# Kernel optimization log

Measured on AMD Instinct MI355X. Metric: run time of the kernel, lower is better.

## Reference

```python
import jax, jax.numpy as jnp
import numpy as np

NUM_GROUPS = 8
K = 2


def setup_inputs() -> dict:
    key = jax.random.key(0)
    k1, k2, k3 = jax.random.split(key, 3)
    b, l, d = 4, 4096, 2048
    g, k = NUM_GROUPS, K
    hdg = d // g  # 256
    x = jax.random.normal(k1, (b, l, d), dtype=jnp.float32)
    Wg = jax.random.normal(k2, (d, g), dtype=jnp.float32) * 0.02  # gate (no bias)
    Wm = jax.random.normal(k3, (k * hdg, k * hdg), dtype=jnp.float32) * 0.02  # inner Linear
    bm = jnp.zeros((k * hdg,), dtype=jnp.float32)
    return {"x": x, "Wg": Wg, "Wm": Wm, "bm": bm}


def reference(x, Wg, Wm, bm):
    b, l, d = x.shape
    g, k = NUM_GROUPS, K
    hdg = d // g
    # gate: softmax + topk over groups
    S = jax.nn.softmax(x @ Wg, axis=-1)            # [b, l, g]
    G, I = jax.lax.top_k(S, k)                     # [b, l, k] each
    x4 = x.reshape(b, l, g, hdg)
    # gather selected feature groups
    sel = jnp.take_along_axis(x4, I[..., None], axis=2)  # [b, l, k, hdg]
    h = (G[..., None] * sel).reshape(b, l, k * hdg)
    # inner model (Linear)
    h = h @ Wm + bm
    h = h.reshape(b, l, k, hdg)
    # scatter back into original groups
    bi = jnp.arange(b)[:, None, None]
    li = jnp.arange(l)[None, :, None]
    out = x4.at[bi, li, I].set(h)
    return out.reshape(b, l, d)
```

## Files before the change

kernel.cpp:

```cpp
#include <hip/hip_runtime.h>
#include <hip/hip_bf16.h>

#define NTOK   16384
#define DIM    2048
#define NGRP   8
#define HDG    256
#define NIN    512

typedef float f32x4 __attribute__((ext_vector_type(4)));
typedef short bf16x8 __attribute__((ext_vector_type(8)));

static __device__ __forceinline__ unsigned short f2bf(float f) {
    unsigned int u = __builtin_bit_cast(unsigned int, f);
    u = (u + 0x7fffu + ((u >> 16) & 1u)) >> 16;
    return (unsigned short)u;
}

__global__ __launch_bounds__(256) void prep_wm(const float* __restrict__ Wm,
                                               ushort* __restrict__ WmT) {
    __shared__ float tile[64][65];
    const int bk = blockIdx.x * 64;
    const int bn = blockIdx.y * 64;
    const int t = threadIdx.x;
    const int r = t >> 4;
    const int c = (t & 15) * 4;
#pragma unroll
    for (int i = 0; i < 4; i++) {
        const float4 v = *(const float4*)&Wm[(bk + r + i * 16) * 512 + bn + c];
        tile[r + i * 16][c + 0] = v.x;
        tile[r + i * 16][c + 1] = v.y;
        tile[r + i * 16][c + 2] = v.z;
        tile[r + i * 16][c + 3] = v.w;
    }
    __syncthreads();
#pragma unroll
    for (int i = 0; i < 4; i++) {
        const int n = r + i * 16;
        ushort4 o;
        o.x = f2bf(tile[c + 0][n]);
        o.y = f2bf(tile[c + 1][n]);
        o.z = f2bf(tile[c + 2][n]);
        o.w = f2bf(tile[c + 3][n]);
        *(ushort4*)&WmT[(bn + n) * 512 + bk + c] = o;
    }
}

__global__ __launch_bounds__(256) void gate_kernel(
        const float* __restrict__ x, const float* __restrict__ Wg,
        int* __restrict__ Isel, float* __restrict__ gvals) {
    const int t = threadIdx.x;
    const int lane = t & 63;
    const int wave = t >> 6;
    const int tok0 = blockIdx.x * 8;

    __shared__ float red[8][4][8];

    float wgr[8][8];
#pragma unroll
    for (int j = 0; j < 8; j++) {
        const float4 a = *(const float4*)&Wg[(t * 8 + j) * 8];
        const float4 b = *(const float4*)&Wg[(t * 8 + j) * 8 + 4];
        wgr[j][0] = a.x; wgr[j][1] = a.y; wgr[j][2] = a.z; wgr[j][3] = a.w;
        wgr[j][4] = b.x; wgr[j][5] = b.y; wgr[j][6] = b.z; wgr[j][7] = b.w;
    }

    int4 xa[3][2];
#pragma unroll
    for (int p = 0; p < 2; p++) {
        xa[p][0] = *(const int4*)&x[(tok0 + p) * DIM + t * 8];
        xa[p][1] = *(const int4*)&x[(tok0 + p) * DIM + t * 8 + 4];
    }

    const bool s0 = lane & 1;
    const bool s1 = lane & 2;
    const bool s2 = lane & 4;

#pragma unroll
    for (int tt = 0; tt < 8; tt++) {
        const int slot = tt % 3;
        const float* xr = (const float*)&xa[slot][0];
        float acc[8];
#pragma unroll
        for (int g = 0; g < 8; g++) acc[g] = 0.f;
#pragma unroll
        for (int j = 0; j < 8; j++)
#pragma unroll
            for (int g = 0; g < 8; g++)
                acc[g] = fmaf(xr[j], wgr[j][g], acc[g]);
        if (tt + 2 < 8) {
            const int ps = (tt + 2) % 3;
            xa[ps][0] = *(const int4*)&x[(tok0 + tt + 2) * DIM + t * 8];
            xa[ps][1] = *(const int4*)&x[(tok0 + tt + 2) * DIM + t * 8 + 4];
        }
        float n_[4];
#pragma unroll
        for (int j = 0; j < 4; j++) {
            const float keep = s0 ? acc[2 * j + 1] : acc[2 * j];
            const float send = s0 ? acc[2 * j] : acc[2 * j + 1];
            n_[j] = keep + __shfl_xor(send, 1, 64);
        }
        float m_[2];
#pragma unroll
        for (int j = 0; j < 2; j++) {
            const float keep = s1 ? n_[2 * j + 1] : n_[2 * j];
            const float send = s1 ? n_[2 * j] : n_[2 * j + 1];
            m_[j] = keep + __shfl_xor(send, 2, 64);
        }
        float v;
        {
            const float keep = s2 ? m_[1] : m_[0];
            const float send = s2 ? m_[0] : m_[1];
            v = keep + __shfl_xor(send, 4, 64);
        }
        v += __shfl_xor(v, 8, 64);
        v += __shfl_xor(v, 16, 64);
        v += __shfl_xor(v, 32, 64);
        if (lane < 8) red[tt][wave][lane] = v;
    }
    __syncthreads();

    const int ll = lane & 31;
    const int tok_local = wave * 2 + (lane >> 5);

    float v = red[tok_local][ll >> 3][ll & 7];
    v += __shfl_xor(v, 8, 64);
    v += __shfl_xor(v, 16, 64);
    float c[8];
    c[0] = v;
    c[1] = __shfl_xor(c[0], 1, 64);
    c[2] = __shfl_xor(c[0], 2, 64);
    c[3] = __shfl_xor(c[1], 2, 64);
    c[4] = __shfl_xor(c[0], 4, 64);
    c[5] = __shfl_xor(c[1], 4, 64);
    c[6] = __shfl_xor(c[2], 4, 64);
    c[7] = __shfl_xor(c[3], 4, 64);
    const int gbase = ll & 7;

    float m = c[0];
#pragma unroll
    for (int j = 1; j < 8; j++) m = fmaxf(m, c[j]);
    float sum = 0.f;
#pragma unroll
    for (int j = 0; j < 8; j++) sum += __expf(c[j] - m);
    int i0 = 8; float v0 = -3.4e38f;
#pragma unroll
    for (int j = 0; j < 8; j++) {
        const int g = gbase ^ j;
        if (c[j] > v0 || (c[j] == v0 && g < i0)) { v0 = c[j]; i0 = g; }
    }
    int i1 = 8; float v1 = -3.4e38f;
#pragma unroll
    for (int j = 0; j < 8; j++) {
        const int g = gbase ^ j;
        if (g != i0 && (c[j] > v1 || (c[j] == v1 && g < i1))) { v1 = c[j]; i1 = g; }
    }
    const float inv = 1.0f / sum;
    if (ll == 0) {
        const int tok = tok0 + tok_local;
        int2 sp; sp.x = i0; sp.y = i1;
        *(int2*)&Isel[tok * 2] = sp;
        float2 gp; gp.x = __expf(v0 - m) * inv; gp.y = __expf(v1 - m) * inv;
        *(float2*)&gvals[tok * 2] = gp;
    }
}

__global__ __launch_bounds__(256) void scatter_copy(
        const float* __restrict__ x, const int* __restrict__ Isel,
        const float* __restrict__ gvals, float* __restrict__ out,
        ushort* __restrict__ hbuf) {
    const int wave = threadIdx.x >> 6;
    const int lane = threadIdx.x & 63;
    const int tok = blockIdx.x * 4 + wave;
    const int2 sel = *(const int2*)&Isel[tok * 2];
    const float2 gv = *(const float2*)&gvals[tok * 2];
    float4 v[8];
#pragma unroll
    for (int j = 0; j < 8; j++)
        v[j] = *(const float4*)&x[tok * DIM + j * HDG + lane * 4];
#pragma unroll
    for (int j = 0; j < 8; j++) {
        if (j == sel.x || j == sel.y) {
            const float g = (j == sel.x) ? gv.x : gv.y;
            const int slot = (j == sel.x) ? 0 : 1;
            int2 pk;
            pk.x = (int)f2bf(g * v[j].x) | ((int)f2bf(g * v[j].y) << 16);
            pk.y = (int)f2bf(g * v[j].z) | ((int)f2bf(g * v[j].w) << 16);
            *(int2*)&hbuf[tok * NIN + slot * HDG + lane * 4] = pk;
        } else {
            *(float4*)&out[tok * DIM + j * HDG + lane * 4] = v[j];
        }
    }
}

__global__ __launch_bounds__(256) void gemm_scatter(
        const ushort* __restrict__ h, const ushort* __restrict__ WmT,
        const float* __restrict__ bm, const int* __restrict__ Isel,
        float* __restrict__ out) {
    __shared__ ushort Hs[2][128][40];
    __shared__ ushort Ws[2][128][40];
    const int t = threadIdx.x;
    const int lane = t & 63;
    const int wave = t >> 6;
    const int wn = (wave >> 1) * 64;
    const int wt = (wave & 1) * 64;
    const int n_blk = blockIdx.x * 128;
    const int tok_blk = blockIdx.y * 128;

    const int sr = t >> 2;
    const int sc = (t & 3) * 8;

    const ushort* hp0 = &h[(tok_blk + sr) * 512 + sc];
    const ushort* hp1 = hp0 + 64 * 512;
    const ushort* wp0 = &WmT[(n_blk + sr) * 512 + sc];
    const ushort* wp1 = wp0 + 64 * 512;

    int4 rh0[3], rh1[3], rw0[3], rw1[3];
#pragma unroll
    for (int p = 0; p < 2; p++) {
        const int off = p * 32;
        rh0[p] = *(const int4*)(hp0 + off);
        rh1[p] = *(const int4*)(hp1 + off);
        rw0[p] = *(const int4*)(wp0 + off);
        rw1[p] = *(const int4*)(wp1 + off);
    }

    f32x4 acc[4][4];
#pragma unroll
    for (int i = 0; i < 4; i++)
#pragma unroll
        for (int j = 0; j < 4; j++)
            acc[i][j] = (f32x4){0.f, 0.f, 0.f, 0.f};

    const int fr = lane & 15;
    const int kh = (lane >> 4) * 8;

#pragma unroll
    for (int k = 0; k < 16; ++k) {
        const int b = k & 1;
        const int s = k % 3;
        *(int4*)&Hs[b][sr][sc]      = rh0[s];
        *(int4*)&Hs[b][sr + 64][sc] = rh1[s];
        *(int4*)&Ws[b][sr][sc]      = rw0[s];
        *(int4*)&Ws[b][sr + 64][sc] = rw1[s];
        __syncthreads();
        if (k + 2 < 16) {
            const int s2 = (k + 2) % 3;
            const int off = (k + 2) * 32;
            rh0[s2] = *(const int4*)(hp0 + off);
            rh1[s2] = *(const int4*)(hp1 + off);
            rw0[s2] = *(const int4*)(wp0 + off);
            rw1[s2] = *(const int4*)(wp1 + off);
        }
        bf16x8 av[4], bv[4];
#pragma unroll
        for (int i = 0; i < 4; i++) av[i] = *(const bf16x8*)&Ws[b][wn + i * 16 + fr][kh];
#pragma unroll
        for (int j = 0; j < 4; j++) bv[j] = *(const bf16x8*)&Hs[b][wt + j * 16 + fr][kh];
#pragma unroll
        for (int i = 0; i < 4; i++)
#pragma unroll
            for (int j = 0; j < 4; j++)
                acc[i][j] = __builtin_amdgcn_mfma_f32_16x16x32_bf16(
                    av[i], bv[j], acc[i][j], 0, 0, 0);
    }

    const int rq = (lane >> 4) * 4;
    const int n_base = n_blk + wn;
    const int s = n_base >> 8;
    const int n_off_base = (n_base & 255) + rq;
    float4 bmv[4];
#pragma unroll
    for (int i = 0; i < 4; i++) bmv[i] = *(const float4*)&bm[n_base + i * 16 + rq];
#pragma unroll
    for (int j = 0; j < 4; j++) {
        const int tok = tok_blk + wt + j * 16 + fr;
        const int2 sel = *(const int2*)&Isel[tok * 2];
        const int grp = s ? sel.y : sel.x;
        float* op = &out[tok * DIM + grp * HDG + n_off_base];
#pragma unroll
        for (int i = 0; i < 4; i++) {
            float4 o;
            o.x = acc[i][j][0] + bmv[i].x;
            o.y = acc[i][j][1] + bmv[i].y;
            o.z = acc[i][j][2] + bmv[i].z;
            o.w = acc[i][j][3] + bmv[i].w;
            *(float4*)&op[i * 16] = o;
        }
    }
}

extern "C" void kernel_launch(void* const* d_in, const int* in_sizes, int n_in,
                              void* d_out, int out_size, void* d_ws, size_t ws_size,
                              hipStream_t stream) {
    const float* x  = (const float*)d_in[0];
    const float* Wg = (const float*)d_in[1];
    const float* Wm = (const float*)d_in[2];
    const float* bm = (const float*)d_in[3];
    float* out = (float*)d_out;

    char* ws = (char*)d_ws;
    ushort* hbuf  = (ushort*)ws;
    ushort* WmT   = (ushort*)(ws + (size_t)16 * 1024 * 1024);
    int*    Isel  = (int*)  (ws + (size_t)16 * 1024 * 1024 + 512 * 1024);
    float*  gvals = (float*)(ws + (size_t)16 * 1024 * 1024 + 640 * 1024);

    prep_wm<<<dim3(8, 8), 256, 0, stream>>>(Wm, WmT);
    gate_kernel<<<NTOK / 8, 256, 0, stream>>>(x, Wg, Isel, gvals);
    scatter_copy<<<NTOK / 4, 256, 0, stream>>>(x, Isel, gvals, out, hbuf);
    gemm_scatter<<<dim3(NIN / 128, NTOK / 128), 256, 0, stream>>>(hbuf, WmT, bm, Isel, out);
}
```

Measured before the change: 320.6 us.

## Fuse passthrough copy into gate kernel and gather-scale inside GEMM

The gate kernel now writes every x row to the output while it already holds it in registers, and the separate scatter/copy kernel is removed. The GEMM now gathers the selected feature groups straight from x, applies the gate weight and converts to bf16 before staging to shared memory, so the intermediate bf16 h buffer is gone. This saves one full read of x and the write and read of h, at the cost of the GEMM re-reading fp32 x once per N-block (four times) and doing extra conversion work in its load path. Launch bounds now ask for two blocks per CU.

After: 299.1 us. 1.07x faster.

```diff
diff --git a/kernel.cpp b/kernel.cpp
--- a/kernel.cpp
+++ b/kernel.cpp
@@ -14,6 +14,9 @@
     unsigned int u = __builtin_bit_cast(unsigned int, f);
     u = (u + 0x7fffu + ((u >> 16) & 1u)) >> 16;
     return (unsigned short)u;
+}
+static __device__ __forceinline__ int pk2(float a, float b) {
+    return (int)f2bf(a) | ((int)f2bf(b) << 16);
 }
 
 __global__ __launch_bounds__(256) void prep_wm(const float* __restrict__ Wm,
@@ -45,9 +48,10 @@
     }
 }
 
-__global__ __launch_bounds__(256) void gate_kernel(
+__global__ __launch_bounds__(256) void gate_copy(
         const float* __restrict__ x, const float* __restrict__ Wg,
-        int* __restrict__ Isel, float* __restrict__ gvals) {
+        float* __restrict__ out, int* __restrict__ Isel,
+        float* __restrict__ gvals) {
     const int t = threadIdx.x;
     const int lane = t & 63;
     const int wave = t >> 6;
@@ -87,6 +91,8 @@
 #pragma unroll
             for (int g = 0; g < 8; g++)
                 acc[g] = fmaf(xr[j], wgr[j][g], acc[g]);
+        *(float4*)&out[(tok0 + tt) * DIM + t * 8]     = *(const float4*)&xr[0];
+        *(float4*)&out[(tok0 + tt) * DIM + t * 8 + 4] = *(const float4*)&xr[4];
         if (tt + 2 < 8) {
             const int ps = (tt + 2) % 3;
             xa[ps][0] = *(const int4*)&x[(tok0 + tt + 2) * DIM + t * 8];
@@ -164,38 +170,10 @@
     }
 }
 
-__global__ __launch_bounds__(256) void scatter_copy(
-        const float* __restrict__ x, const int* __restrict__ Isel,
-        const float* __restrict__ gvals, float* __restrict__ out,
-        ushort* __restrict__ hbuf) {
-    const int wave = threadIdx.x >> 6;
-    const int lane = threadIdx.x & 63;
-    const int tok = blockIdx.x * 4 + wave;
-    const int2 sel = *(const int2*)&Isel[tok * 2];
-    const float2 gv = *(const float2*)&gvals[tok * 2];
-    float4 v[8];
-#pragma unroll
-    for (int j = 0; j < 8; j++)
-        v[j] = *(const float4*)&x[tok * DIM + j * HDG + lane * 4];
-#pragma unroll
-    for (int j = 0; j < 8; j++) {
-        if (j == sel.x || j == sel.y) {
-            const float g = (j == sel.x) ? gv.x : gv.y;
-            const int slot = (j == sel.x) ? 0 : 1;
-            int2 pk;
-            pk.x = (int)f2bf(g * v[j].x) | ((int)f2bf(g * v[j].y) << 16);
-            pk.y = (int)f2bf(g * v[j].z) | ((int)f2bf(g * v[j].w) << 16);
-            *(int2*)&hbuf[tok * NIN + slot * HDG + lane * 4] = pk;
-        } else {
-            *(float4*)&out[tok * DIM + j * HDG + lane * 4] = v[j];
-        }
-    }
-}
-
-__global__ __launch_bounds__(256) void gemm_scatter(
-        const ushort* __restrict__ h, const ushort* __restrict__ WmT,
+__global__ __launch_bounds__(256, 2) void gemm_scatter(
+        const float* __restrict__ x, const ushort* __restrict__ WmT,
         const float* __restrict__ bm, const int* __restrict__ Isel,
-        float* __restrict__ out) {
+        const float* __restrict__ gvals, float* __restrict__ out) {
     __shared__ ushort Hs[2][128][40];
     __shared__ ushort Ws[2][128][40];
     const int t = threadIdx.x;
@@ -209,17 +187,31 @@
     const int sr = t >> 2;
     const int sc = (t & 3) * 8;
 
-    const ushort* hp0 = &h[(tok_blk + sr) * 512 + sc];
-    const ushort* hp1 = hp0 + 64 * 512;
+    const int tokA = tok_blk + sr;
+    const int tokB = tokA + 64;
+    const int2 selA = *(const int2*)&Isel[tokA * 2];
+    const int2 selB = *(const int2*)&Isel[tokB * 2];
+    const float2 gvA = *(const float2*)&gvals[tokA * 2];
+    const float2 gvB = *(const float2*)&gvals[tokB * 2];
+    const float* xA[2] = { &x[tokA * DIM + selA.x * HDG + sc],
+                           &x[tokA * DIM + selA.y * HDG + sc] };
+    const float* xB[2] = { &x[tokB * DIM + selB.x * HDG + sc],
+                           &x[tokB * DIM + selB.y * HDG + sc] };
+    const float gA[2] = { gvA.x, gvA.y };
+    const float gB[2] = { gvB.x, gvB.y };
+
     const ushort* wp0 = &WmT[(n_blk + sr) * 512 + sc];
     const ushort* wp1 = wp0 + 64 * 512;
 
-    int4 rh0[3], rh1[3], rw0[3], rw1[3];
+    float4 fA[3][2], fB[3][2];
+    int4 rw0[3], rw1[3];
 #pragma unroll
     for (int p = 0; p < 2; p++) {
         const int off = p * 32;
-        rh0[p] = *(const int4*)(hp0 + off);
-        rh1[p] = *(const int4*)(hp1 + off);
+        fA[p][0] = *(const float4*)(xA[0] + off);
+        fA[p][1] = *(const float4*)(xA[0] + off + 4);
+        fB[p][0] = *(const float4*)(xB[0] + off);
+        fB[p][1] = *(const float4*)(xB[0] + off + 4);
         rw0[p] = *(const int4*)(wp0 + off);
         rw1[p] = *(const int4*)(wp1 + off);
     }
@@ -238,18 +230,32 @@
     for (int k = 0; k < 16; ++k) {
         const int b = k & 1;
         const int s = k % 3;
-        *(int4*)&Hs[b][sr][sc]      = rh0[s];
-        *(int4*)&Hs[b][sr + 64][sc] = rh1[s];
+        const float ga = gA[k >> 3];
+        const float gb = gB[k >> 3];
+        int4 wa, wb;
+        wa.x = pk2(fA[s][0].x * ga, fA[s][0].y * ga);
+        wa.y = pk2(fA[s][0].z * ga, fA[s][0].w * ga);
+        wa.z = pk2(fA[s][1].x * ga, fA[s][1].y * ga);
+        wa.w = pk2(fA[s][1].z * ga, fA[s][1].w * ga);
+        wb.x = pk2(fB[s][0].x * gb, fB[s][0].y * gb);
+        wb.y = pk2(fB[s][0].z * gb, fB[s][0].w * gb);
+        wb.z = pk2(fB[s][1].x * gb, fB[s][1].y * gb);
+        wb.w = pk2(fB[s][1].z * gb, fB[s][1].w * gb);
+        *(int4*)&Hs[b][sr][sc]      = wa;
+        *(int4*)&Hs[b][sr + 64][sc] = wb;
         *(int4*)&Ws[b][sr][sc]      = rw0[s];
         *(int4*)&Ws[b][sr + 64][sc] = rw1[s];
         __syncthreads();
         if (k + 2 < 16) {
             const int s2 = (k + 2) % 3;
-            const int off = (k + 2) * 32;
-            rh0[s2] = *(const int4*)(hp0 + off);
-            rh1[s2] = *(const int4*)(hp1 + off);
-            rw0[s2] = *(const int4*)(wp0 + off);
-            rw1[s2] = *(const int4*)(wp1 + off);
+            const int slot2 = (k + 2) >> 3;
+            const int off = ((k + 2) & 7) * 32;
+            fA[s2][0] = *(const float4*)(xA[slot2] + off);
+            fA[s2][1] = *(const float4*)(xA[slot2] + off + 4);
+            fB[s2][0] = *(const float4*)(xB[slot2] + off);
+            fB[s2][1] = *(const float4*)(xB[slot2] + off + 4);
+            rw0[s2] = *(const int4*)(wp0 + (k + 2) * 32);
+            rw1[s2] = *(const int4*)(wp1 + (k + 2) * 32);
         }
         bf16x8 av[4], bv[4];
 #pragma unroll
@@ -299,13 +305,11 @@
     float* out = (float*)d_out;
 
     char* ws = (char*)d_ws;
-    ushort* hbuf  = (ushort*)ws;
-    ushort* WmT   = (ushort*)(ws + (size_t)16 * 1024 * 1024);
-    int*    Isel  = (int*)  (ws + (size_t)16 * 1024 * 1024 + 512 * 1024);
-    float*  gvals = (float*)(ws + (size_t)16 * 1024 * 1024 + 640 * 1024);
+    ushort* WmT   = (ushort*)ws;
+    int*    Isel  = (int*)  (ws + 512 * 1024);
+    float*  gvals = (float*)(ws + 640 * 1024);
 
     prep_wm<<<dim3(8, 8), 256, 0, stream>>>(Wm, WmT);
-    gate_kernel<<<NTOK / 8, 256, 0, stream>>>(x, Wg, Isel, gvals);
-    scatter_copy<<<NTOK / 4, 256, 0, stream>>>(x, Isel, gvals, out, hbuf);
-    gemm_scatter<<<dim3(NIN / 128, NTOK / 128), 256, 0, stream>>>(hbuf, WmT, bm, Isel, out);
-}
+    gate_copy<<<NTOK / 8, 256, 0, stream>>>(x, Wg, out, Isel, gvals);
+    gemm_scatter<<<dim3(NIN / 128, NTOK / 128), 256, 0, stream>>>(x, WmT, bm, Isel, gvals, out);
+}
```
